# Performance work log

Hardware: AMD Instinct MI355X
Metric: run time of the kernel (lower is better)

## Reference

```python
import jax, jax.numpy as jnp
import numpy as np

N = 64       # HiPPO order
L = 1024     # sequence length (= max_length)
BATCH = 2048 # batch size


def _legs_AB(n):
    """Canonical HiPPO-LegS transition matrices (GuTransMatrix with defaults).
    A[i,k] = -sqrt(2i+1)sqrt(2k+1) for i>k, -(i+1) for i==k, 0 for i<k.
    B[i]   = sqrt(2i+1).
    """
    q = np.arange(n, dtype=np.float64)
    r = np.sqrt(2.0 * q + 1.0)
    M = r[:, None] * r[None, :]
    A = -np.where(q[:, None] > q[None, :], M, 0.0) - np.diag(q + 1.0)
    return A.astype(np.float32), r.astype(np.float32)


def _stack_bilinear(A, Bv, length):
    """Per-step bilinear (Tustin, alpha=0.5) discretization of A/t, B/t."""
    n = A.shape[0]
    I = np.eye(n, dtype=np.float32)
    A_st = np.empty((length, n, n), dtype=np.float32)
    B_st = np.empty((length, n), dtype=np.float32)
    for t in range(1, length + 1):
        At = A / t
        lhs = I - 0.5 * At
        A_st[t - 1] = np.linalg.solve(lhs, I + 0.5 * At)
        B_st[t - 1] = np.linalg.solve(lhs, Bv / t)
    return A_st, B_st


def setup_inputs() -> dict:
    key = jax.random.key(0)
    A, Bv = _legs_AB(N)
    A_st, B_st = _stack_bilinear(A, Bv, L)
    inputs = jax.random.normal(key, (L, BATCH), dtype=jnp.float32)
    return {
        "inputs": inputs,
        "A_stacked": jnp.asarray(A_st),  # (L, N, N)
        "B_stacked": jnp.asarray(B_st),  # (L, N)
    }


def reference(inputs, A_stacked, B_stacked):
    # u[t, b, :] = inputs[t, b] * B_stacked[t]  -> (L, B, N)
    u = inputs[..., None] * B_stacked[:, None, :]

    def step(c, xs):
        A_t, u_t = xs                 # (N, N), (B, N)
        c = u_t + c @ A_t.T           # c_t = A_t @ c_{t-1} + B_t * f_t
        return c, c

    c0 = jnp.zeros(u.shape[1:], dtype=u.dtype)  # (B, N)
    _, cs = jax.lax.scan(step, c0, (A_stacked, u))
    return cs  # (L, B, N)
```

## Files before the change

kernel.cpp:

```cpp
#include <hip/hip_runtime.h>
#include <hip/hip_fp16.h>

#define L_SEQ  1024
#define NBATCH 2048
#define NSTATE 64
#define TCHK   64
#define NCHK   16
#define KDIM   128

typedef _Float16 half8  __attribute__((ext_vector_type(8)));
typedef _Float16 half2s __attribute__((ext_vector_type(2)));
typedef float    float4v __attribute__((ext_vector_type(4)));
typedef unsigned int uint2v __attribute__((ext_vector_type(2)));
typedef unsigned int uint4v __attribute__((ext_vector_type(4)));

__global__ __launch_bounds__(256) void split_A_kernel(const float* __restrict__ A,
                                                      _Float16* __restrict__ hi,
                                                      _Float16* __restrict__ lo) {
    int i = blockIdx.x * 256 + threadIdx.x;
    float a = A[i];
    _Float16 h = (_Float16)a;
    hi[i] = h;
    lo[i] = (_Float16)(a - (float)h);
}

__global__ __launch_bounds__(256) void zero_G_kernel(float4v* __restrict__ p) {
    size_t i = (size_t)blockIdx.x * 256 + threadIdx.x;
    p[i] = float4v{0.0f, 0.0f, 0.0f, 0.0f};
}

__global__ __launch_bounds__(64, 1) void build_G_kernel(
    const _Float16* __restrict__ Ahi,
    const _Float16* __restrict__ Alo,
    const float* __restrict__ bst,
    _Float16* __restrict__ Ghi,
    _Float16* __restrict__ Glo)
{
    const int lane = threadIdx.x;
    const int col  = lane & 15;
    const int quad = lane >> 4;
    const int chunk = blockIdx.x >> 3;
    const int ct    = blockIdx.x & 7;
    const int swz  = (col & 7) << 2;

    __shared__ unsigned int u_hi[1024];
    __shared__ unsigned int u_lo[1024];
    for (int i = lane; i < 1024; i += 64) { u_hi[i] = 0u; u_lo[i] = 0u; }
    if (ct < 4 && lane < 16) {
        int c = ct * 16 + lane;
        u_hi[lane * 32 + (((c >> 1) & 31) ^ ((lane & 7) << 2))] =
            (c & 1) ? 0x3C000000u : 0x00003C00u;
    }

    int aoff[4][2];
#pragma unroll
    for (int tl = 0; tl < 4; ++tl)
#pragma unroll
        for (int kk = 0; kk < 2; ++kk)
            aoff[tl][kk] = (16 * tl + col) * 64 + 32 * kk + 8 * quad;

    half8 aH0[4][2], aL0[4][2], aH1[4][2], aL1[4][2];
    float4v bs0[4], bs1[4];

    auto loadA = [&](int i, half8 (&aH)[4][2], half8 (&aL)[4][2], float4v (&bs)[4]) {
        size_t base = (size_t)(chunk * TCHK + i) * 4096;
#pragma unroll
        for (int tl = 0; tl < 4; ++tl) {
#pragma unroll
            for (int kk = 0; kk < 2; ++kk) {
                aH[tl][kk] = *(const half8*)(Ahi + base + aoff[tl][kk]);
                aL[tl][kk] = *(const half8*)(Alo + base + aoff[tl][kk]);
            }
            bs[tl] = *(const float4v*)(bst + (chunk * TCHK + i) * NSTATE + 16 * tl + 4 * quad);
        }
    };

    loadA(0, aH0, aL0, bs0);
    loadA(1, aH1, aL1, bs1);

    const float4v zero4 = {0.0f, 0.0f, 0.0f, 0.0f};

    auto stepG = [&](int i, half8 (&aH)[4][2], half8 (&aL)[4][2], float4v (&bs)[4]) {
        const int cur = (i & 1) << 9;
        const int nxt = cur ^ 512;
        const int lim = 64 + i;
        const int inj_ct = lim >> 4, inj_c = lim & 15;

        if (ct * 16 <= lim) {
            int rowb = cur + col * 32;
            uint4v uh0 = *(const uint4v*)(u_hi + rowb + (( 0 + 4 * quad) ^ swz));
            uint4v uh1 = *(const uint4v*)(u_hi + rowb + ((16 + 4 * quad) ^ swz));
            uint4v ul0 = *(const uint4v*)(u_lo + rowb + (( 0 + 4 * quad) ^ swz));
            uint4v ul1 = *(const uint4v*)(u_lo + rowb + ((16 + 4 * quad) ^ swz));
            half8 ch0 = __builtin_bit_cast(half8, uh0), ch1 = __builtin_bit_cast(half8, uh1);
            half8 cl0 = __builtin_bit_cast(half8, ul0), cl1 = __builtin_bit_cast(half8, ul1);

#pragma unroll
            for (int tl = 0; tl < 4; ++tl) {
                float4v a = zero4;
                a = __builtin_amdgcn_mfma_f32_16x16x32_f16(aH[tl][0], ch0, a, 0, 0, 0);
                a = __builtin_amdgcn_mfma_f32_16x16x32_f16(aH[tl][1], ch1, a, 0, 0, 0);
                a = __builtin_amdgcn_mfma_f32_16x16x32_f16(aH[tl][0], cl0, a, 0, 0, 0);
                a = __builtin_amdgcn_mfma_f32_16x16x32_f16(aH[tl][1], cl1, a, 0, 0, 0);
                a = __builtin_amdgcn_mfma_f32_16x16x32_f16(aL[tl][0], ch0, a, 0, 0, 0);
                a = __builtin_amdgcn_mfma_f32_16x16x32_f16(aL[tl][1], ch1, a, 0, 0, 0);
                if (ct == inj_ct && col == inj_c) a += bs[tl];

                _Float16 hx = (_Float16)a.x, hy = (_Float16)a.y;
                _Float16 hz = (_Float16)a.z, hw = (_Float16)a.w;
                _Float16 lx = (_Float16)(a.x - (float)hx), ly = (_Float16)(a.y - (float)hy);
                _Float16 lz = (_Float16)(a.z - (float)hz), lw = (_Float16)(a.w - (float)hw);
                half2s hp01; hp01.x = hx; hp01.y = hy;
                half2s hp23; hp23.x = hz; hp23.y = hw;
                half2s lp01; lp01.x = lx; lp01.y = ly;
                half2s lp23; lp23.x = lz; lp23.y = lw;
                uint2v hp = { __builtin_bit_cast(unsigned int, hp01), __builtin_bit_cast(unsigned int, hp23) };
                uint2v lp = { __builtin_bit_cast(unsigned int, lp01), __builtin_bit_cast(unsigned int, lp23) };
                *(uint2v*)(u_hi + nxt + col * 32 + ((8 * tl + 2 * quad) ^ swz)) = hp;
                *(uint2v*)(u_lo + nxt + col * 32 + ((8 * tl + 2 * quad) ^ swz)) = lp;

                size_t grow = ((size_t)(chunk * TCHK + i) * NSTATE + 16 * tl + 4 * quad) * KDIM + ct * 16 + col;
                Ghi[grow          ] = hx; Glo[grow          ] = lx;
                Ghi[grow +     KDIM] = hy; Glo[grow +     KDIM] = ly;
                Ghi[grow + 2 * KDIM] = hz; Glo[grow + 2 * KDIM] = lz;
                Ghi[grow + 3 * KDIM] = hw; Glo[grow + 3 * KDIM] = lw;
            }
        }
        int tp = i + 2; if (tp > TCHK - 1) tp = TCHK - 1;
        loadA(tp, aH, aL, bs);
    };

    for (int i = 0; i < TCHK; i += 2) {
        stepG(i,     aH0, aL0, bs0);
        stepG(i + 1, aH1, aL1, bs1);
    }
}

__global__ __launch_bounds__(256, 1) void boundary2_kernel(
    const float* __restrict__ inp,
    const _Float16* __restrict__ Ghi,
    const _Float16* __restrict__ Glo,
    unsigned int* __restrict__ s_hi,
    unsigned int* __restrict__ s_lo)
{
    const int tid  = threadIdx.x;
    const int lane = tid & 63;
    const int wave = tid >> 6;
    const int col  = lane & 15;
    const int quad = lane >> 4;
    const int b0   = blockIdx.x * 64;
    const int b    = b0 + wave * 16 + col;
    const int swz  = (col & 7) << 2;

    __shared__ _Float16 gstage[2][2][64][128];
    __shared__ float    istage[2][64][64];
    __shared__ unsigned int cst[4][2][512];

    for (int i = lane; i < 512; i += 64) { cst[wave][0][i] = 0u; cst[wave][1][i] = 0u; }
    {
        const uint4v z4 = {0u, 0u, 0u, 0u};
        size_t sb = ((size_t)b) * 32 + 8 * quad;
        *(uint4v*)(s_hi + sb) = z4; *(uint4v*)(s_hi + sb + 4) = z4;
        *(uint4v*)(s_lo + sb) = z4; *(uint4v*)(s_lo + sb + 4) = z4;
    }

    half8  gr[8];
    float4v ir[4];
    auto stage_issue = [&](int k) {
        size_t base = (size_t)(k * TCHK + 63) * NSTATE * KDIM;
#pragma unroll
        for (int j = 0; j < 8; ++j) {
            int off = j * 2048 + tid * 8;
            gr[j] = (off < 8192) ? *(const half8*)(Ghi + base + off)
                                 : *(const half8*)(Glo + base + off - 8192);
        }
#pragma unroll
        for (int q2 = 0; q2 < 4; ++q2) {
            int fi   = q2 * 256 + tid;
            int tloc = fi >> 4;
            int f4   = fi & 15;
            ir[q2] = *(const float4v*)(inp + (size_t)(k * TCHK + tloc) * NBATCH + b0 + f4 * 4);
        }
    };
    auto stage_write = [&](int buf) {
#pragma unroll
        for (int j = 0; j < 8; ++j) {
            int off = j * 2048 + tid * 8;
            int reg = off >> 13;
            int loff = off & 8191;
            int row = loff >> 7;
            int c   = (loff & 127) ^ ((row & 7) << 3);
            *(half8*)&gstage[buf][reg][row][c] = gr[j];
        }
#pragma unroll
        for (int q2 = 0; q2 < 4; ++q2) {
            int fi   = q2 * 256 + tid;
            int tloc = fi >> 4;
            int f4   = fi & 15;
            *(float4v*)&istage[buf][tloc][f4 * 4] = ir[q2];
        }
    };

    const float4v zero4 = {0.0f, 0.0f, 0.0f, 0.0f};

    stage_issue(0);
    stage_write(0);
    __syncthreads();

    for (int k = 0; k < NCHK; ++k) {
        const int cur = k & 1;
        if (k < NCHK - 1) stage_issue(k + 1);

        uint4v uh0 = *(const uint4v*)(cst[wave][0] + col * 32 + (( 0 + 4 * quad) ^ swz));
        uint4v uh1 = *(const uint4v*)(cst[wave][0] + col * 32 + ((16 + 4 * quad) ^ swz));
        uint4v ul0 = *(const uint4v*)(cst[wave][1] + col * 32 + (( 0 + 4 * quad) ^ swz));
        uint4v ul1 = *(const uint4v*)(cst[wave][1] + col * 32 + ((16 + 4 * quad) ^ swz));
        half8 xh[4], xl[4];
        xh[0] = __builtin_bit_cast(half8, uh0); xh[1] = __builtin_bit_cast(half8, uh1);
        xl[0] = __builtin_bit_cast(half8, ul0); xl[1] = __builtin_bit_cast(half8, ul1);
#pragma unroll
        for (int kk2 = 0; kk2 < 2; ++kk2) {
            half8 h, l;
#pragma unroll
            for (int e = 0; e < 8; ++e) {
                float v = istage[cur][kk2 * 32 + 8 * quad + e][wave * 16 + col];
                _Float16 hh = (_Float16)v;
                h[e] = hh; l[e] = (_Float16)(v - (float)hh);
            }
            xh[2 + kk2] = h; xl[2 + kk2] = l;
        }

        float4v acc[4];
#pragma unroll
        for (int tl = 0; tl < 4; ++tl) {
            float4v a = zero4;
#pragma unroll
            for (int kk = 0; kk < 4; ++kk) {
                const int row = 16 * tl + col;
                const int c   = (32 * kk + 8 * quad) ^ ((col & 7) << 3);
                half8 gh = *(const half8*)&gstage[cur][0][row][c];
                half8 gl = *(const half8*)&gstage[cur][1][row][c];
                a = __builtin_amdgcn_mfma_f32_16x16x32_f16(gh, xh[kk], a, 0, 0, 0);
                a = __builtin_amdgcn_mfma_f32_16x16x32_f16(gh, xl[kk], a, 0, 0, 0);
                a = __builtin_amdgcn_mfma_f32_16x16x32_f16(gl, xh[kk], a, 0, 0, 0);
            }
            acc[tl] = a;
        }

        if (k < NCHK - 1) {
#pragma unroll
            for (int tl = 0; tl < 4; ++tl) {
                float4v a = acc[tl];
                _Float16 hx = (_Float16)a.x, hy = (_Float16)a.y;
                _Float16 hz = (_Float16)a.z, hw = (_Float16)a.w;
                _Float16 lx = (_Float16)(a.x - (float)hx), ly = (_Float16)(a.y - (float)hy);
                _Float16 lz = (_Float16)(a.z - (float)hz), lw = (_Float16)(a.w - (float)hw);
                half2s hp01; hp01.x = hx; hp01.y = hy;
                half2s hp23; hp23.x = hz; hp23.y = hw;
                half2s lp01; lp01.x = lx; lp01.y = ly;
                half2s lp23; lp23.x = lz; lp23.y = lw;
                uint2v hp = { __builtin_bit_cast(unsigned int, hp01), __builtin_bit_cast(unsigned int, hp23) };
                uint2v lp = { __builtin_bit_cast(unsigned int, lp01), __builtin_bit_cast(unsigned int, lp23) };
                *(uint2v*)(cst[wave][0] + col * 32 + ((8 * tl + 2 * quad) ^ swz)) = hp;
                *(uint2v*)(cst[wave][1] + col * 32 + ((8 * tl + 2 * quad) ^ swz)) = lp;
                size_t sb = ((size_t)(k + 1) * NBATCH + b) * 32 + 8 * tl + 2 * quad;
                *(uint2v*)(s_hi + sb) = hp;
                *(uint2v*)(s_lo + sb) = lp;
            }
            stage_write(cur ^ 1);
        }
        __syncthreads();
    }
}

__global__ __launch_bounds__(256, 1) void apply2_kernel(
    const float* __restrict__ inp,
    const _Float16* __restrict__ Ghi,
    const _Float16* __restrict__ Glo,
    const unsigned int* __restrict__ s_hi,
    const unsigned int* __restrict__ s_lo,
    float* __restrict__ out)
{
    const int tid  = threadIdx.x;
    const int lane = tid & 63;
    const int wave = tid >> 6;
    const int col  = lane & 15;
    const int quad = lane >> 4;

    const int virt  = (blockIdx.x & 7) * 256 + (blockIdx.x >> 3);
    const int chunk = virt >> 7;
    const int ig    = (virt >> 4) & 7;
    const int bt    = virt & 15;

    __shared__ _Float16 gbuf[2][2][16][64][8];

    int bb[2];
    bb[0] = bt * 128 + wave * 32 + col;
    bb[1] = bb[0] + 16;
    half8 xh[2][4], xl[2][4];
#pragma unroll
    for (int bs = 0; bs < 2; ++bs) {
        size_t sb = ((size_t)chunk * NBATCH + bb[bs]) * 32;
        uint4v sh0 = *(const uint4v*)(s_hi + sb +  0 + 4 * quad);
        uint4v sh1 = *(const uint4v*)(s_hi + sb + 16 + 4 * quad);
        uint4v sl0 = *(const uint4v*)(s_lo + sb +  0 + 4 * quad);
        uint4v sl1 = *(const uint4v*)(s_lo + sb + 16 + 4 * quad);
        xh[bs][0] = __builtin_bit_cast(half8, sh0); xh[bs][1] = __builtin_bit_cast(half8, sh1);
        xl[bs][0] = __builtin_bit_cast(half8, sl0); xl[bs][1] = __builtin_bit_cast(half8, sl1);
#pragma unroll
        for (int kk2 = 0; kk2 < 2; ++kk2) {
            half8 h, l;
#pragma unroll
            for (int e = 0; e < 8; ++e) {
                float v = inp[(size_t)(chunk * TCHK + kk2 * 32 + 8 * quad + e) * NBATCH + bb[bs]];
                _Float16 hh = (_Float16)v;
                h[e] = hh; l[e] = (_Float16)(v - (float)hh);
            }
            xh[bs][2 + kk2] = h; xl[bs][2 + kk2] = l;
        }
    }

    half8 sreg[8];
    auto stage_issue = [&](int i) {
        size_t base = ((size_t)(chunk * TCHK + ig * 8 + i) * NSTATE + 16 * wave + col) * KDIM + 8 * quad;
#pragma unroll
        for (int kk = 0; kk < 4; ++kk) {
            sreg[kk * 2 + 0] = *(const half8*)(Ghi + base + 32 * kk);
            sreg[kk * 2 + 1] = *(const half8*)(Glo + base + 32 * kk);
        }
    };
    auto stage_write = [&](int buf) {
#pragma unroll
        for (int kk = 0; kk < 4; ++kk) {
            *(half8*)&gbuf[buf][0][wave * 4 + kk][lane][0] = sreg[kk * 2 + 0];
            *(half8*)&gbuf[buf][1][wave * 4 + kk][lane][0] = sreg[kk * 2 + 1];
        }
    };

    const float4v zero4 = {0.0f, 0.0f, 0.0f, 0.0f};
    float4v* outv = (float4v*)out;

    stage_issue(0);
    stage_write(0);
    __syncthreads();

    for (int i = 0; i < 8; ++i) {
        const int cur = i & 1;
        if (i < 7) stage_issue(i + 1);

        float4v acc[2][4];
#pragma unroll
        for (int bs = 0; bs < 2; ++bs)
#pragma unroll
            for (int tl = 0; tl < 4; ++tl) acc[bs][tl] = zero4;

#pragma unroll
        for (int kk = 0; kk < 4; ++kk) {
            half8 gh[4], gl[4];
#pragma unroll
            for (int tl = 0; tl < 4; ++tl) {
                gh[tl] = *(const half8*)&gbuf[cur][0][tl * 4 + kk][lane][0];
                gl[tl] = *(const half8*)&gbuf[cur][1][tl * 4 + kk][lane][0];
            }
#pragma unroll
            for (int tl = 0; tl < 4; ++tl) {
#pragma unroll
                for (int bs = 0; bs < 2; ++bs) {
                    acc[bs][tl] = __builtin_amdgcn_mfma_f32_16x16x32_f16(gh[tl], xh[bs][kk], acc[bs][tl], 0, 0, 0);
                    acc[bs][tl] = __builtin_amdgcn_mfma_f32_16x16x32_f16(gh[tl], xl[bs][kk], acc[bs][tl], 0, 0, 0);
                    acc[bs][tl] = __builtin_amdgcn_mfma_f32_16x16x32_f16(gl[tl], xh[bs][kk], acc[bs][tl], 0, 0, 0);
                }
            }
        }

        const size_t tt = (size_t)(chunk * TCHK + ig * 8 + i);
#pragma unroll
        for (int bs = 0; bs < 2; ++bs)
#pragma unroll
            for (int tl = 0; tl < 4; ++tl)
                outv[(tt * NBATCH + bb[bs]) * 16 + 4 * tl + quad] = acc[bs][tl];

        if (i < 7) stage_write(cur ^ 1);
        __syncthreads();
    }
}

template <bool USE_WS>
__global__ __launch_bounds__(64, 1) void hippo_scan_kernel(
    const float* __restrict__ inp, const float* __restrict__ bst,
    const float* __restrict__ A32, const _Float16* __restrict__ Ahi,
    const _Float16* __restrict__ Alo, float* __restrict__ out)
{
    const int lane = threadIdx.x;
    const int col  = lane & 15;
    const int quad = lane >> 4;
    const int b0   = blockIdx.x * 16;
    const int swz  = (col & 7) << 2;

    __shared__ unsigned int c_hi[1024];
    __shared__ unsigned int c_lo[1024];
    for (int i = lane; i < 1024; i += 64) { c_hi[i] = 0u; c_lo[i] = 0u; }

    const int rd0 = col * 32 + (( 0 + 4 * quad) ^ swz);
    const int rd1 = col * 32 + ((16 + 4 * quad) ^ swz);
    int wr[4];
#pragma unroll
    for (int ts = 0; ts < 4; ++ts) wr[ts] = col * 32 + ((8 * ts + 2 * quad) ^ swz);

    int aoff[4][2];
#pragma unroll
    for (int tl = 0; tl < 4; ++tl)
#pragma unroll
        for (int kk = 0; kk < 2; ++kk)
            aoff[tl][kk] = (16 * tl + col) * 64 + 32 * kk + 8 * quad;

    half8 ah0[4][2], al0[4][2], ah1[4][2], al1[4][2];
    float inp0, inp1;
    float4v bst0[4], bst1[4];

    auto load_set = [&](int t, half8 (&ah)[4][2], half8 (&al)[4][2],
                        float4v (&bstv)[4], float& inpv) {
#pragma unroll
        for (int tl = 0; tl < 4; ++tl) {
#pragma unroll
            for (int kk = 0; kk < 2; ++kk) {
                if constexpr (USE_WS) {
                    ah[tl][kk] = *(const half8*)(Ahi + (size_t)t * 4096 + aoff[tl][kk]);
                    al[tl][kk] = *(const half8*)(Alo + (size_t)t * 4096 + aoff[tl][kk]);
                } else {
                    const float* p = A32 + (size_t)t * 4096 + aoff[tl][kk];
                    float4v f0 = *(const float4v*)(p);
                    float4v f1 = *(const float4v*)(p + 4);
                    half8 h, l;
#pragma unroll
                    for (int e = 0; e < 4; ++e) {
                        float v0 = f0[e], v1 = f1[e];
                        _Float16 h0 = (_Float16)v0, h1 = (_Float16)v1;
                        h[e] = h0; h[e + 4] = h1;
                        l[e] = (_Float16)(v0 - (float)h0);
                        l[e + 4] = (_Float16)(v1 - (float)h1);
                    }
                    ah[tl][kk] = h; al[tl][kk] = l;
                }
            }
        }
        inpv = inp[t * NBATCH + b0 + col];
#pragma unroll
        for (int tl = 0; tl < 4; ++tl)
            bstv[tl] = *(const float4v*)(bst + t * NSTATE + 16 * tl + 4 * quad);
    };

    load_set(0, ah0, al0, bst0, inp0);
    load_set(1, ah1, al1, bst1, inp1);
    const float4v zero4 = {0.0f, 0.0f, 0.0f, 0.0f};

    auto step = [&](int t, int cur, half8 (&ah)[4][2], half8 (&al)[4][2],
                    float4v (&bstv)[4], float& inpv) {
        const int nxt = cur ^ 512;
        uint4v u_h0 = *(const uint4v*)(c_hi + cur + rd0);
        uint4v u_h1 = *(const uint4v*)(c_hi + cur + rd1);
        uint4v u_l0 = *(const uint4v*)(c_lo + cur + rd0);
        uint4v u_l1 = *(const uint4v*)(c_lo + cur + rd1);
        half8 ch[2] = { __builtin_bit_cast(half8, u_h0), __builtin_bit_cast(half8, u_h1) };
        half8 cl[2] = { __builtin_bit_cast(half8, u_l0), __builtin_bit_cast(half8, u_l1) };

        float4v acc[4];
#pragma unroll
        for (int tl = 0; tl < 4; ++tl) {
            float4v accA = bstv[tl] * inpv;
            accA = __builtin_amdgcn_mfma_f32_16x16x32_f16(ah[tl][0], ch[0], accA, 0, 0, 0);
            accA = __builtin_amdgcn_mfma_f32_16x16x32_f16(ah[tl][1], ch[1], accA, 0, 0, 0);
            float4v accB = __builtin_amdgcn_mfma_f32_16x16x32_f16(ah[tl][0], cl[0], zero4, 0, 0, 0);
            accB = __builtin_amdgcn_mfma_f32_16x16x32_f16(ah[tl][1], cl[1], accB, 0, 0, 0);
            accB = __builtin_amdgcn_mfma_f32_16x16x32_f16(al[tl][0], ch[0], accB, 0, 0, 0);
            accB = __builtin_amdgcn_mfma_f32_16x16x32_f16(al[tl][1], ch[1], accB, 0, 0, 0);
            acc[tl] = accA + accB;
        }

        float4v* outv = (float4v*)out;
#pragma unroll
        for (int tl = 0; tl < 4; ++tl)
            outv[(size_t)(t * NBATCH + b0 + col) * 16 + 4 * tl + quad] = acc[tl];

        int tp = t + 2; if (tp > L_SEQ - 1) tp = L_SEQ - 1;
        load_set(tp, ah, al, bstv, inpv);

#pragma unroll
        for (int tl = 0; tl < 4; ++tl) {
            float x = acc[tl].x, y = acc[tl].y, z = acc[tl].z, w = acc[tl].w;
            _Float16 hx = (_Float16)x, hy = (_Float16)y, hz = (_Float16)z, hw = (_Float16)w;
            half2s hp01; hp01.x = hx; hp01.y = hy;
            half2s hp23; hp23.x = hz; hp23.y = hw;
            half2s lp01; lp01.x = (_Float16)(x - (float)hx); lp01.y = (_Float16)(y - (float)hy);
            half2s lp23; lp23.x = (_Float16)(z - (float)hz); lp23.y = (_Float16)(w - (float)hw);
            uint2v hp = { __builtin_bit_cast(unsigned int, hp01), __builtin_bit_cast(unsigned int, hp23) };
            uint2v lp = { __builtin_bit_cast(unsigned int, lp01), __builtin_bit_cast(unsigned int, lp23) };
            *(uint2v*)(c_hi + nxt + wr[tl]) = hp;
            *(uint2v*)(c_lo + nxt + wr[tl]) = lp;
        }
    };

    for (int t = 0; t < L_SEQ; t += 2) {
        step(t,     0,   ah0, al0, bst0, inp0);
        step(t + 1, 512, ah1, al1, bst1, inp1);
    }
}

extern "C" void kernel_launch(void* const* d_in, const int* in_sizes, int n_in,
                              void* d_out, int out_size, void* d_ws, size_t ws_size,
                              hipStream_t stream) {
    const float* inputs = (const float*)d_in[0];
    const float* A_st   = (const float*)d_in[1];
    const float* B_st   = (const float*)d_in[2];
    float* out = (float*)d_out;

    const size_t n_a    = (size_t)L_SEQ * NSTATE * NSTATE;
    const size_t SZ_A   = n_a * sizeof(_Float16);
    const size_t SZ_G   = (size_t)NCHK * TCHK * NSTATE * KDIM * sizeof(_Float16);
    const size_t SZ_S   = (size_t)NCHK * NBATCH * 32 * sizeof(unsigned int);
    const size_t OFF_ALO = SZ_A;
    const size_t OFF_GHI = 2 * SZ_A;
    const size_t OFF_GLO = OFF_GHI + SZ_G;
    const size_t OFF_SHI = OFF_GLO + SZ_G;
    const size_t OFF_SLO = OFF_SHI + SZ_S;
    const size_t NEED    = OFF_SLO + SZ_S;

    if (ws_size >= NEED) {
        char* ws = (char*)d_ws;
        _Float16* Ahi = (_Float16*)ws;
        _Float16* Alo = (_Float16*)(ws + OFF_ALO);
        _Float16* Ghi = (_Float16*)(ws + OFF_GHI);
        _Float16* Glo = (_Float16*)(ws + OFF_GLO);
        unsigned int* shi = (unsigned int*)(ws + OFF_SHI);
        unsigned int* slo = (unsigned int*)(ws + OFF_SLO);

        split_A_kernel<<<(int)(n_a / 256), 256, 0, stream>>>(A_st, Ahi, Alo);
        zero_G_kernel<<<(int)(2 * SZ_G / 16 / 256), 256, 0, stream>>>((float4v*)(ws + OFF_GHI));
        build_G_kernel<<<NCHK * 8, 64, 0, stream>>>(Ahi, Alo, B_st, Ghi, Glo);
        boundary2_kernel<<<NBATCH / 64, 256, 0, stream>>>(inputs, Ghi, Glo, shi, slo);
        apply2_kernel<<<NCHK * 8 * 16, 256, 0, stream>>>(inputs, Ghi, Glo, shi, slo, out);
    } else if (ws_size >= 2 * SZ_A) {
        _Float16* Ahi = (_Float16*)d_ws;
        _Float16* Alo = Ahi + n_a;
        split_A_kernel<<<(int)(n_a / 256), 256, 0, stream>>>(A_st, Ahi, Alo);
        hippo_scan_kernel<true><<<NBATCH / 16, 64, 0, stream>>>(inputs, B_st, A_st, Ahi, Alo, out);
    } else {
        hippo_scan_kernel<false><<<NBATCH / 16, 64, 0, stream>>>(inputs, B_st, A_st, nullptr, nullptr, out);
    }
}
```

Measured before the change: 271.7 us.

## Split build_G row tiles across four waves with block barriers

The G-building kernel moves from one wave handling all four 16-row tiles of the 64x64 recurrence step to four waves, each owning one row tile, with a block barrier after each step to publish the shared-memory state. This shortens the serial per-step chain of MFMAs and stores in one wave and spreads the A-tile register and load pressure across waves. The cost is a __syncthreads per time step and four times as many threads in only 128 blocks, so barrier latency may eat much of the gain on this serial prologue.

New measurement: 276.8 us. About the same (+1.9%).

```diff
diff --git a/kernel.cpp b/kernel.cpp
--- a/kernel.cpp
+++ b/kernel.cpp
@@ -29,14 +29,16 @@
     p[i] = float4v{0.0f, 0.0f, 0.0f, 0.0f};
 }
 
-__global__ __launch_bounds__(64, 1) void build_G_kernel(
+__global__ __launch_bounds__(256, 1) void build_G_kernel(
     const _Float16* __restrict__ Ahi,
     const _Float16* __restrict__ Alo,
     const float* __restrict__ bst,
     _Float16* __restrict__ Ghi,
     _Float16* __restrict__ Glo)
 {
-    const int lane = threadIdx.x;
+    const int tid  = threadIdx.x;
+    const int lane = tid & 63;
+    const int tl   = tid >> 6;
     const int col  = lane & 15;
     const int quad = lane >> 4;
     const int chunk = blockIdx.x >> 3;
@@ -45,34 +47,28 @@
 
     __shared__ unsigned int u_hi[1024];
     __shared__ unsigned int u_lo[1024];
-    for (int i = lane; i < 1024; i += 64) { u_hi[i] = 0u; u_lo[i] = 0u; }
-    if (ct < 4 && lane < 16) {
-        int c = ct * 16 + lane;
-        u_hi[lane * 32 + (((c >> 1) & 31) ^ ((lane & 7) << 2))] =
+    for (int i = tid; i < 1024; i += 256) { u_hi[i] = 0u; u_lo[i] = 0u; }
+    __syncthreads();
+    if (ct < 4 && tid < 16) {
+        int c = ct * 16 + tid;
+        u_hi[tid * 32 + (((c >> 1) & 31) ^ ((tid & 7) << 2))] =
             (c & 1) ? 0x3C000000u : 0x00003C00u;
     }
-
-    int aoff[4][2];
-#pragma unroll
-    for (int tl = 0; tl < 4; ++tl)
-#pragma unroll
-        for (int kk = 0; kk < 2; ++kk)
-            aoff[tl][kk] = (16 * tl + col) * 64 + 32 * kk + 8 * quad;
-
-    half8 aH0[4][2], aL0[4][2], aH1[4][2], aL1[4][2];
-    float4v bs0[4], bs1[4];
-
-    auto loadA = [&](int i, half8 (&aH)[4][2], half8 (&aL)[4][2], float4v (&bs)[4]) {
+    __syncthreads();
+
+    const int aoff0 = (16 * tl + col) * 64 +  0 + 8 * quad;
+    const int aoff1 = (16 * tl + col) * 64 + 32 + 8 * quad;
+
+    half8 aH0[2], aL0[2], aH1[2], aL1[2];
+    float4v bs0, bs1;
+
+    auto loadA = [&](int i, half8 (&aH)[2], half8 (&aL)[2], float4v& bs) {
         size_t base = (size_t)(chunk * TCHK + i) * 4096;
-#pragma unroll
-        for (int tl = 0; tl < 4; ++tl) {
-#pragma unroll
-            for (int kk = 0; kk < 2; ++kk) {
-                aH[tl][kk] = *(const half8*)(Ahi + base + aoff[tl][kk]);
-                aL[tl][kk] = *(const half8*)(Alo + base + aoff[tl][kk]);
-            }
-            bs[tl] = *(const float4v*)(bst + (chunk * TCHK + i) * NSTATE + 16 * tl + 4 * quad);
-        }
+        aH[0] = *(const half8*)(Ahi + base + aoff0);
+        aH[1] = *(const half8*)(Ahi + base + aoff1);
+        aL[0] = *(const half8*)(Alo + base + aoff0);
+        aL[1] = *(const half8*)(Alo + base + aoff1);
+        bs = *(const float4v*)(bst + (chunk * TCHK + i) * NSTATE + 16 * tl + 4 * quad);
     };
 
     loadA(0, aH0, aL0, bs0);
@@ -80,7 +76,7 @@
 
     const float4v zero4 = {0.0f, 0.0f, 0.0f, 0.0f};
 
-    auto stepG = [&](int i, half8 (&aH)[4][2], half8 (&aL)[4][2], float4v (&bs)[4]) {
+    auto stepG = [&](int i, half8 (&aH)[2], half8 (&aL)[2], float4v& bs) {
         const int cur = (i & 1) << 9;
         const int nxt = cur ^ 512;
         const int lim = 64 + i;
@@ -95,39 +91,37 @@
             half8 ch0 = __builtin_bit_cast(half8, uh0), ch1 = __builtin_bit_cast(half8, uh1);
             half8 cl0 = __builtin_bit_cast(half8, ul0), cl1 = __builtin_bit_cast(half8, ul1);
 
-#pragma unroll
-            for (int tl = 0; tl < 4; ++tl) {
-                float4v a = zero4;
-                a = __builtin_amdgcn_mfma_f32_16x16x32_f16(aH[tl][0], ch0, a, 0, 0, 0);
-                a = __builtin_amdgcn_mfma_f32_16x16x32_f16(aH[tl][1], ch1, a, 0, 0, 0);
-                a = __builtin_amdgcn_mfma_f32_16x16x32_f16(aH[tl][0], cl0, a, 0, 0, 0);
-                a = __builtin_amdgcn_mfma_f32_16x16x32_f16(aH[tl][1], cl1, a, 0, 0, 0);
-                a = __builtin_amdgcn_mfma_f32_16x16x32_f16(aL[tl][0], ch0, a, 0, 0, 0);
-                a = __builtin_amdgcn_mfma_f32_16x16x32_f16(aL[tl][1], ch1, a, 0, 0, 0);
-                if (ct == inj_ct && col == inj_c) a += bs[tl];
-
-                _Float16 hx = (_Float16)a.x, hy = (_Float16)a.y;
-                _Float16 hz = (_Float16)a.z, hw = (_Float16)a.w;
-                _Float16 lx = (_Float16)(a.x - (float)hx), ly = (_Float16)(a.y - (float)hy);
-                _Float16 lz = (_Float16)(a.z - (float)hz), lw = (_Float16)(a.w - (float)hw);
-                half2s hp01; hp01.x = hx; hp01.y = hy;
-                half2s hp23; hp23.x = hz; hp23.y = hw;
-                half2s lp01; lp01.x = lx; lp01.y = ly;
-                half2s lp23; lp23.x = lz; lp23.y = lw;
-                uint2v hp = { __builtin_bit_cast(unsigned int, hp01), __builtin_bit_cast(unsigned int, hp23) };
-                uint2v lp = { __builtin_bit_cast(unsigned int, lp01), __builtin_bit_cast(unsigned int, lp23) };
-                *(uint2v*)(u_hi + nxt + col * 32 + ((8 * tl + 2 * quad) ^ swz)) = hp;
-                *(uint2v*)(u_lo + nxt + col * 32 + ((8 * tl + 2 * quad) ^ swz)) = lp;
-
-                size_t grow = ((size_t)(chunk * TCHK + i) * NSTATE + 16 * tl + 4 * quad) * KDIM + ct * 16 + col;
-                Ghi[grow          ] = hx; Glo[grow          ] = lx;
-                Ghi[grow +     KDIM] = hy; Glo[grow +     KDIM] = ly;
-                Ghi[grow + 2 * KDIM] = hz; Glo[grow + 2 * KDIM] = lz;
-                Ghi[grow + 3 * KDIM] = hw; Glo[grow + 3 * KDIM] = lw;
-            }
+            float4v a = zero4;
+            a = __builtin_amdgcn_mfma_f32_16x16x32_f16(aH[0], ch0, a, 0, 0, 0);
+            a = __builtin_amdgcn_mfma_f32_16x16x32_f16(aH[1], ch1, a, 0, 0, 0);
+            a = __builtin_amdgcn_mfma_f32_16x16x32_f16(aH[0], cl0, a, 0, 0, 0);
+            a = __builtin_amdgcn_mfma_f32_16x16x32_f16(aH[1], cl1, a, 0, 0, 0);
+            a = __builtin_amdgcn_mfma_f32_16x16x32_f16(aL[0], ch0, a, 0, 0, 0);
+            a = __builtin_amdgcn_mfma_f32_16x16x32_f16(aL[1], ch1, a, 0, 0, 0);
+            if (ct == inj_ct && col == inj_c) a += bs;
+
+            _Float16 hx = (_Float16)a.x, hy = (_Float16)a.y;
+            _Float16 hz = (_Float16)a.z, hw = (_Float16)a.w;
+            _Float16 lx = (_Float16)(a.x - (float)hx), ly = (_Float16)(a.y - (float)hy);
+            _Float16 lz = (_Float16)(a.z - (float)hz), lw = (_Float16)(a.w - (float)hw);
+            half2s hp01; hp01.x = hx; hp01.y = hy;
+            half2s hp23; hp23.x = hz; hp23.y = hw;
+            half2s lp01; lp01.x = lx; lp01.y = ly;
+            half2s lp23; lp23.x = lz; lp23.y = lw;
+            uint2v hp = { __builtin_bit_cast(unsigned int, hp01), __builtin_bit_cast(unsigned int, hp23) };
+            uint2v lp = { __builtin_bit_cast(unsigned int, lp01), __builtin_bit_cast(unsigned int, lp23) };
+            *(uint2v*)(u_hi + nxt + col * 32 + ((8 * tl + 2 * quad) ^ swz)) = hp;
+            *(uint2v*)(u_lo + nxt + col * 32 + ((8 * tl + 2 * quad) ^ swz)) = lp;
+
+            size_t grow = ((size_t)(chunk * TCHK + i) * NSTATE + 16 * tl + 4 * quad) * KDIM + ct * 16 + col;
+            Ghi[grow          ] = hx; Glo[grow          ] = lx;
+            Ghi[grow +     KDIM] = hy; Glo[grow +     KDIM] = ly;
+            Ghi[grow + 2 * KDIM] = hz; Glo[grow + 2 * KDIM] = lz;
+            Ghi[grow + 3 * KDIM] = hw; Glo[grow + 3 * KDIM] = lw;
         }
         int tp = i + 2; if (tp > TCHK - 1) tp = TCHK - 1;
         loadA(tp, aH, aL, bs);
+        __syncthreads();
     };
 
     for (int i = 0; i < TCHK; i += 2) {
@@ -536,7 +530,7 @@
 
         split_A_kernel<<<(int)(n_a / 256), 256, 0, stream>>>(A_st, Ahi, Alo);
         zero_G_kernel<<<(int)(2 * SZ_G / 16 / 256), 256, 0, stream>>>((float4v*)(ws + OFF_GHI));
-        build_G_kernel<<<NCHK * 8, 64, 0, stream>>>(Ahi, Alo, B_st, Ghi, Glo);
+        build_G_kernel<<<NCHK * 8, 256, 0, stream>>>(Ahi, Alo, B_st, Ghi, Glo);
         boundary2_kernel<<<NBATCH / 64, 256, 0, stream>>>(inputs, Ghi, Glo, shi, slo);
         apply2_kernel<<<NCHK * 8 * 16, 256, 0, stream>>>(inputs, Ghi, Glo, shi, slo, out);
     } else if (ws_size >= 2 * SZ_A) {
```
